# Kernel tuning notes

Measured on AMD Instinct MI355X. Metric: run time of the kernel, lower is better.

## Reference

```python
import jax, jax.numpy as jnp
import numpy as np

N = 100000   # nodes
E = 1600000  # edges
F_IN = 256   # nfeat
H = 64       # hidden_sizes
C = 40       # nclass


def gcn_norm(edge_index, edge_weight, num_nodes):
    # Add self-loops with weight 1 (PyG gcn_norm default fill_value=1.0)
    loop = jnp.arange(num_nodes)
    row = jnp.concatenate([edge_index[0], loop])
    col = jnp.concatenate([edge_index[1], loop])
    w = jnp.concatenate([edge_weight, jnp.ones((num_nodes,), edge_weight.dtype)])
    # Symmetric normalization: D^-1/2 A D^-1/2 (degree computed at target, per PyG)
    deg = jax.ops.segment_sum(w, col, num_segments=num_nodes)
    deg_inv_sqrt = jnp.where(deg > 0, jax.lax.rsqrt(deg), 0.0)
    norm = deg_inv_sqrt[row] * w * deg_inv_sqrt[col]
    return row, col, norm


def gcn_conv(x, W, b, row, col, norm, num_nodes):
    # Linear transform first (shrinks feature dim before irregular traffic)
    x = x @ W                                    # [N, out]
    msgs = norm[:, None] * x[row]                # gather + scale: [E+N, out]
    out = jax.ops.segment_sum(msgs, col, num_segments=num_nodes)  # scatter-add
    return out + b


def setup_inputs() -> dict:
    key = jax.random.key(0)
    k = jax.random.split(key, 7)
    x = jax.random.normal(k[0], (N, F_IN), dtype=jnp.float32)
    edge_index = jax.random.randint(k[1], (2, E), 0, N, dtype=jnp.int64)
    edge_attr = jax.random.uniform(k[2], (E,), dtype=jnp.float32)
    W1 = jax.random.normal(k[3], (F_IN, H), dtype=jnp.float32) * (1.0 / np.sqrt(F_IN))
    b1 = jnp.zeros((H,), jnp.float32)
    W2 = jax.random.normal(k[4], (H, C), dtype=jnp.float32) * (1.0 / np.sqrt(H))
    b2 = jnp.zeros((C,), jnp.float32)
    return {"x": x, "edge_index": edge_index, "edge_attr": edge_attr,
            "W1": W1, "b1": b1, "W2": W2, "b2": b2}


def reference(x, edge_index, edge_attr, W1, b1, W2, b2):
    row, col, norm = gcn_norm(edge_index, edge_attr, N)
    h = jax.nn.relu(gcn_conv(x, W1, b1, row, col, norm, N))
    # F.dropout with training=False is identity (eval mode)
    final = gcn_conv(h, W2, b2, row, col, norm, N)
    return final, jax.nn.log_softmax(final, axis=1)
```

## Files before the change

### kernel.cpp

```cpp
#include <hip/hip_runtime.h>
#include <hip/hip_bf16.h>
#include <math.h>

#define NN 100000
#define EE 1600000
#define FIN 256
#define HID 64
#define NC 40
#define NB 196
#define BCAP 10240
#define CHUNK 2048
#define NBKB ((EE + CHUNK - 1) / CHUNK)

typedef unsigned long long ull;
typedef __attribute__((ext_vector_type(2))) unsigned long long ullx2;
typedef __attribute__((ext_vector_type(8))) short short8;
typedef __attribute__((ext_vector_type(4))) float f32x4;

__device__ __forceinline__ unsigned short f2bf_rne(float f) {
    unsigned u = __float_as_uint(f);
    u += 0x7FFFu + ((u >> 16) & 1u);
    return (unsigned short)(u >> 16);
}
__device__ __forceinline__ float bf2f(unsigned short b) {
    return __uint_as_float((unsigned)b << 16);
}

__device__ __forceinline__ void edge_acc(ull q, const unsigned* __restrict__ tbl,
                                         int fl, float& a0, float& a1) {
    unsigned src = (unsigned)q & 0x1FFFFu;
    unsigned u = tbl[(src << 5) | fl];
    float w = __int_as_float((int)(q >> 32));
    a0 += w * __uint_as_float(u << 16);
    a1 += w * __uint_as_float(u & 0xFFFF0000u);
}

__global__ __launch_bounds__(256) void bucket_kernel(const int* __restrict__ row,
                                                     const int* __restrict__ col,
                                                     const float* __restrict__ w,
                                                     int* __restrict__ bucket_cnt,
                                                     int2* __restrict__ staging) {
    __shared__ int2 spay[CHUNK];
    __shared__ int2 sorted[CHUNK];
    __shared__ unsigned char sb[CHUNK];
    __shared__ unsigned char sbk[CHUNK];
    __shared__ int lcnt[NB], lofs[NB], lstart[NB];
    __shared__ int sscan[256];
    const int tid = threadIdx.x;
    const int e0 = blockIdx.x * CHUNK;
    const int nE = min(CHUNK, EE - e0);
    for (int i = tid; i < nE; i += 256) {
        int e = e0 + i;
        int c = col[e];
        sb[i] = (unsigned char)(c >> 9);
        spay[i] = make_int2(((c & 511) << 17) | row[e], __float_as_int(w[e]));
    }
    for (int i = tid; i < NB; i += 256) lcnt[i] = 0;
    __syncthreads();
    for (int i = tid; i < nE; i += 256) atomicAdd(&lcnt[sb[i]], 1);
    __syncthreads();
    int v = (tid < NB) ? lcnt[tid] : 0;
    sscan[tid] = v;
    __syncthreads();
    for (int off = 1; off < 256; off <<= 1) {
        int u = (tid >= off) ? sscan[tid - off] : 0;
        __syncthreads();
        sscan[tid] += u;
        __syncthreads();
    }
    if (tid < NB) {
        lofs[tid] = sscan[tid] - v;
        lstart[tid] = v ? atomicAdd(&bucket_cnt[tid], v) : 0;
        lcnt[tid] = 0;
    }
    __syncthreads();
    for (int i = tid; i < nE; i += 256) {
        int b = sb[i];
        int p = lofs[b] + atomicAdd(&lcnt[b], 1);
        sorted[p] = spay[i];
        sbk[p] = (unsigned char)b;
    }
    __syncthreads();
    for (int p = tid; p < nE; p += 256) {
        int b = sbk[p];
        int slot = lstart[b] + (p - lofs[b]);
        if (slot < BCAP) staging[(size_t)b * BCAP + slot] = sorted[p];
    }
}

__global__ __launch_bounds__(512) void build_count_kernel(const int2* __restrict__ staging,
                                                          const int* __restrict__ bucket_cnt,
                                                          int* __restrict__ basev,
                                                          int* __restrict__ endv,
                                                          float* __restrict__ dis,
                                                          int* __restrict__ ptot) {
    __shared__ int dcnt[512];
    __shared__ float dsum[512];
    __shared__ int sscan[512];
    const int t = threadIdx.x;
    const int b = blockIdx.x;
    const int nE = min(bucket_cnt[b], BCAP);
    const int2* st = staging + (size_t)b * BCAP;
    dcnt[t] = 0; dsum[t] = 0.f;
    __syncthreads();
    for (int i = t; i < nE; i += 512) {
        int2 p = st[i];
        int d = p.x >> 17;
        atomicAdd(&dcnt[d], 1);
        atomicAdd(&dsum[d], __int_as_float(p.y));
    }
    __syncthreads();
    int c = dcnt[t];
    int pdeg = (c + 7) & ~7;
    sscan[t] = pdeg;
    __syncthreads();
    for (int off = 1; off < 512; off <<= 1) {
        int u = (t >= off) ? sscan[t - off] : 0;
        __syncthreads();
        sscan[t] += u;
        __syncthreads();
    }
    int gd = b * 512 + t;
    if (gd < NN) {
        basev[gd] = sscan[t] - pdeg;
        endv[gd] = c;
        dis[gd] = rsqrtf(dsum[t] + 1.0f);
    }
    if (t == 511) ptot[b] = sscan[511];
}

__global__ __launch_bounds__(256) void bscan_w1cvt_kernel(const int* __restrict__ ptot,
                                                          int* __restrict__ bucket_base,
                                                          const float* __restrict__ W1,
                                                          unsigned short* __restrict__ w1hi,
                                                          unsigned short* __restrict__ w1lo) {
    if (blockIdx.x == 0) {
        __shared__ int sd[256];
        int t = threadIdx.x;
        int v = (t < NB) ? ptot[t] : 0;
        sd[t] = v;
        __syncthreads();
        for (int off = 1; off < 256; off <<= 1) {
            int u = (t >= off) ? sd[t - off] : 0;
            __syncthreads();
            sd[t] += u;
            __syncthreads();
        }
        if (t < NB) bucket_base[t] = sd[t] - v;
    } else {
        int b = blockIdx.x - 1;
        for (int i = threadIdx.x; i < 4096; i += 256) {
            int e = b * 4096 + i;
            int c = e >> 8, k = e & 255;
            float v = W1[(size_t)k * HID + c];
            unsigned short h = f2bf_rne(v);
            w1hi[e] = h;
            w1lo[e] = f2bf_rne(v - bf2f(h));
        }
    }
}

__global__ __launch_bounds__(512) void build_place_kernel(const int2* __restrict__ staging,
                                                          const int* __restrict__ bucket_cnt,
                                                          const int* __restrict__ bucket_base,
                                                          int* __restrict__ basev,
                                                          int* __restrict__ endv,
                                                          const float* __restrict__ dis,
                                                          int2* __restrict__ eme) {
    __shared__ int dcur[512];
    __shared__ float sdis[512];
    const int t = threadIdx.x;
    const int b = blockIdx.x;
    const int nE = min(bucket_cnt[b], BCAP);
    const int2* st = staging + (size_t)b * BCAP;
    const int gd = b * 512 + t;
    int gb = 0, c = 0, pdeg = 0;
    if (gd < NN) {
        gb = bucket_base[b] + basev[gd];
        c = endv[gd];
        pdeg = (c + 7) & ~7;
        basev[gd] = gb;
        endv[gd] = gb + c;
        sdis[t] = dis[gd];
    } else {
        sdis[t] = 0.f;
    }
    dcur[t] = gb;
    __syncthreads();
    for (int i = t; i < nE; i += 512) {
        int2 p = st[i];
        int d = p.x >> 17;
        int src = p.x & 0x1FFFF;
        int pos = atomicAdd(&dcur[d], 1);
        float wn = __int_as_float(p.y) * dis[src] * sdis[d];
        eme[pos] = make_int2(src, __float_as_int(wn));
    }
    for (int i = c; i < pdeg; i++) eme[gb + i] = make_int2(0, 0);
}

__global__ __launch_bounds__(512, 4) void gemm1_mfma_kernel(const float* __restrict__ x,
                                                            const unsigned short* __restrict__ w1hi,
                                                            const unsigned short* __restrict__ w1lo,
                                                            __hip_bfloat16* __restrict__ xw) {
    __shared__ unsigned short shi[4096 * 2];
    __shared__ unsigned short slo[4096 * 2];
    const int tid = threadIdx.x;
    const int wid = tid >> 6;
    const int l   = tid & 63;
    const int r   = l & 15;
    const int kg  = l >> 4;
    const int rb0 = blockIdx.x * 128 + wid * 16;

    f32x4 acc[4];
#pragma unroll
    for (int j = 0; j < 4; j++) acc[j] = (f32x4){0.f, 0.f, 0.f, 0.f};

    int row0 = rb0 + r;
    int row0c = row0 < NN ? row0 : NN - 1;
    const float* ap = x + (size_t)row0c * FIN + kg * 8;

#pragma unroll
    for (int ph = 0; ph < 2; ph++) {
        for (int c2 = tid; c2 < 1024; c2 += 512) {
            int ckg = c2 & 3, ccol = (c2 >> 2) & 63, cksl = c2 >> 8;
            size_t src = (size_t)ccol * FIN + (ph * 4 + cksl) * 32 + ckg * 8;
            int dst = ((cksl * 64 + ccol) * 32 + ckg * 8);
            *(short8*)(shi + dst) = *(const short8*)(w1hi + src);
            *(short8*)(slo + dst) = *(const short8*)(w1lo + src);
        }
        __syncthreads();
#pragma unroll
        for (int ksl = 0; ksl < 4; ksl++) {
            const int ks = ph * 4 + ksl;
            float4 afa = *(const float4*)(ap + ks * 32);
            float4 afb = *(const float4*)(ap + ks * 32 + 4);
            float av[8] = {afa.x, afa.y, afa.z, afa.w, afb.x, afb.y, afb.z, afb.w};
            short8 ahi, alo;
#pragma unroll
            for (int j = 0; j < 8; j++) {
                unsigned short hh = f2bf_rne(av[j]);
                ahi[j] = (short)hh;
                alo[j] = (short)f2bf_rne(av[j] - bf2f(hh));
            }
#pragma unroll
            for (int ct = 0; ct < 4; ct++) {
                int bo = ((ksl * 64 + ct * 16 + r) * 32 + kg * 8);
                short8 bh = *(const short8*)(shi + bo);
                short8 bl = *(const short8*)(slo + bo);
                acc[ct] = __builtin_amdgcn_mfma_f32_16x16x32_bf16(ahi, bh, acc[ct], 0, 0, 0);
                acc[ct] = __builtin_amdgcn_mfma_f32_16x16x32_bf16(ahi, bl, acc[ct], 0, 0, 0);
                acc[ct] = __builtin_amdgcn_mfma_f32_16x16x32_bf16(alo, bh, acc[ct], 0, 0, 0);
            }
        }
        __syncthreads();
    }
#pragma unroll
    for (int i = 0; i < 4; i++) {
        int grow = rb0 + kg * 4 + i;
        if (grow < NN) {
            unsigned short* dst = (unsigned short*)xw + (size_t)grow * HID + r;
#pragma unroll
            for (int ct = 0; ct < 4; ct++)
                dst[ct * 16] = f2bf_rne(acc[ct][i]);
        }
    }
}

__global__ __launch_bounds__(256) void gather1_kernel(const int* __restrict__ basev,
                                                      const int* __restrict__ endv,
                                                      const ull* __restrict__ eme,
                                                      const unsigned* __restrict__ xw32,
                                                      const float* __restrict__ dis,
                                                      const float* __restrict__ b,
                                                      float* __restrict__ h) {
    int n = blockIdx.x * 4 + (threadIdx.x >> 6);
    if (n >= NN) return;
    int lane = threadIdx.x & 63;
    int half = lane >> 5;
    int fl = lane & 31;
    int s = basev[n], t = endv[n];
    int pdeg = (t - s + 7) & ~7;
    float acc0 = 0.f, acc1 = 0.f;
    int nb16 = pdeg >> 4;
    for (int bi = 0; bi < nb16; bi++) {
        const ull* pp = eme + s + bi * 16 + 8 * half;
        ullx2 qa = *(const ullx2*)(pp);
        ullx2 qb = *(const ullx2*)(pp + 2);
        ullx2 qc = *(const ullx2*)(pp + 4);
        ullx2 qd = *(const ullx2*)(pp + 6);
        edge_acc(qa[0], xw32, fl, acc0, acc1);
        edge_acc(qa[1], xw32, fl, acc0, acc1);
        edge_acc(qb[0], xw32, fl, acc0, acc1);
        edge_acc(qb[1], xw32, fl, acc0, acc1);
        edge_acc(qc[0], xw32, fl, acc0, acc1);
        edge_acc(qc[1], xw32, fl, acc0, acc1);
        edge_acc(qd[0], xw32, fl, acc0, acc1);
        edge_acc(qd[1], xw32, fl, acc0, acc1);
    }
    if (pdeg & 8) {
        const ull* pp = eme + s + nb16 * 16 + 4 * half;
        ullx2 qa = *(const ullx2*)(pp);
        ullx2 qb = *(const ullx2*)(pp + 2);
        edge_acc(qa[0], xw32, fl, acc0, acc1);
        edge_acc(qa[1], xw32, fl, acc0, acc1);
        edge_acc(qb[0], xw32, fl, acc0, acc1);
        edge_acc(qb[1], xw32, fl, acc0, acc1);
    }
    acc0 += __shfl_xor(acc0, 32);
    acc1 += __shfl_xor(acc1, 32);
    float d = dis[n];
    unsigned un = xw32[((unsigned)n << 5) | fl];
    float2 bv = *(const float2*)(b + 2 * fl);
    float v0 = acc0 + d * d * __uint_as_float(un << 16) + bv.x;
    float v1 = acc1 + d * d * __uint_as_float(un & 0xFFFF0000u) + bv.y;
    if (lane < 32) {
        *(float2*)(h + (size_t)n * HID + 2 * fl) = make_float2(fmaxf(v0, 0.f), fmaxf(v1, 0.f));
    }
}

__global__ __launch_bounds__(256) void gemm2_kernel(const float* __restrict__ h,
                                                    const float* __restrict__ W,
                                                    __hip_bfloat16* __restrict__ hw) {
    __shared__ float hs[64][65];
    __shared__ float Ws[HID * NC];
    const int tid = threadIdx.x;
    const int base = blockIdx.x * 64;
    for (int v = tid; v < 1024; v += 256) {
        int r = v >> 4, q = v & 15;
        int gr = base + r;
        float4 hv = make_float4(0.f, 0.f, 0.f, 0.f);
        if (gr < NN) hv = *(const float4*)(h + (size_t)gr * HID + q * 4);
        hs[r][q * 4 + 0] = hv.x; hs[r][q * 4 + 1] = hv.y;
        hs[r][q * 4 + 2] = hv.z; hs[r][q * 4 + 3] = hv.w;
    }
    for (int v = tid; v < HID * NC; v += 256) Ws[v] = W[v];
    __syncthreads();
    const int tx = tid & 7;
    const int ty = tid >> 3;
    float acc[2][5] = {};
#pragma unroll 8
    for (int k = 0; k < HID; k++) {
        float h0 = hs[ty * 2 + 0][k];
        float h1 = hs[ty * 2 + 1][k];
        const float* wr = &Ws[k * NC + tx * 5];
        float w0 = wr[0], w1 = wr[1], w2 = wr[2], w3 = wr[3], w4 = wr[4];
        acc[0][0] += h0 * w0; acc[0][1] += h0 * w1; acc[0][2] += h0 * w2;
        acc[0][3] += h0 * w3; acc[0][4] += h0 * w4;
        acc[1][0] += h1 * w0; acc[1][1] += h1 * w1; acc[1][2] += h1 * w2;
        acc[1][3] += h1 * w3; acc[1][4] += h1 * w4;
    }
#pragma unroll
    for (int i = 0; i < 2; i++) {
        int gr = base + ty * 2 + i;
        if (gr < NN) {
#pragma unroll
            for (int c = 0; c < 5; c++)
                hw[(size_t)gr * 64 + tx * 5 + c] = __float2bfloat16(acc[i][c]);
        }
    }
}

__global__ __launch_bounds__(256) void gather2_kernel(const int* __restrict__ basev,
                                                      const int* __restrict__ endv,
                                                      const ull* __restrict__ eme,
                                                      const unsigned* __restrict__ hw32,
                                                      const float* __restrict__ dis,
                                                      const float* __restrict__ b,
                                                      float* __restrict__ out) {
    int n = blockIdx.x * 4 + (threadIdx.x >> 6);
    if (n >= NN) return;
    int lane = threadIdx.x & 63;
    int half = lane >> 5;
    int fl = lane & 31;
    bool act = fl < 20;
    int s = basev[n], t = endv[n];
    int pdeg = (t - s + 7) & ~7;
    float acc0 = 0.f, acc1 = 0.f;
    int nb16 = pdeg >> 4;
    for (int bi = 0; bi < nb16; bi++) {
        const ull* pp = eme + s + bi * 16 + 8 * half;
        ullx2 qa = *(const ullx2*)(pp);
        ullx2 qb = *(const ullx2*)(pp + 2);
        ullx2 qc = *(const ullx2*)(pp + 4);
        ullx2 qd = *(const ullx2*)(pp + 6);
        edge_acc(qa[0], hw32, fl, acc0, acc1);
        edge_acc(qa[1], hw32, fl, acc0, acc1);
        edge_acc(qb[0], hw32, fl, acc0, acc1);
        edge_acc(qb[1], hw32, fl, acc0, acc1);
        edge_acc(qc[0], hw32, fl, acc0, acc1);
        edge_acc(qc[1], hw32, fl, acc0, acc1);
        edge_acc(qd[0], hw32, fl, acc0, acc1);
        edge_acc(qd[1], hw32, fl, acc0, acc1);
    }
    if (pdeg & 8) {
        const ull* pp = eme + s + nb16 * 16 + 4 * half;
        ullx2 qa = *(const ullx2*)(pp);
        ullx2 qb = *(const ullx2*)(pp + 2);
        edge_acc(qa[0], hw32, fl, acc0, acc1);
        edge_acc(qa[1], hw32, fl, acc0, acc1);
        edge_acc(qb[0], hw32, fl, acc0, acc1);
        edge_acc(qb[1], hw32, fl, acc0, acc1);
    }
    acc0 += __shfl_xor(acc0, 32);
    acc1 += __shfl_xor(acc1, 32);
    float v0 = 0.f, v1 = 0.f, m = -INFINITY;
    if (act) {
        float d = dis[n];
        unsigned un = hw32[((unsigned)n << 5) | fl];
        float2 bv = *(const float2*)(b + 2 * fl);
        v0 = acc0 + d * d * __uint_as_float(un << 16) + bv.x;
        v1 = acc1 + d * d * __uint_as_float(un & 0xFFFF0000u) + bv.y;
        m = fmaxf(v0, v1);
    }
#pragma unroll
    for (int off = 16; off; off >>= 1) m = fmaxf(m, __shfl_xor(m, off));
    float e0 = act ? expf(v0 - m) : 0.f;
    float e1 = act ? expf(v1 - m) : 0.f;
    float sum = e0 + e1;
#pragma unroll
    for (int off = 16; off; off >>= 1) sum += __shfl_xor(sum, off);
    float lse = m + logf(sum);
    if (act && lane < 32) {
        size_t idx = (size_t)n * NC + 2 * fl;
        *(float2*)(out + idx) = make_float2(v0, v1);
        *(float2*)(out + (size_t)NN * NC + idx) = make_float2(v0 - lse, v1 - lse);
    }
}

extern "C" void kernel_launch(void* const* d_in, const int* in_sizes, int n_in,
                              void* d_out, int out_size, void* d_ws, size_t ws_size,
                              hipStream_t stream) {
    const float* x    = (const float*)d_in[0];
    const int*   eidx = (const int*)d_in[1];
    const float* ew   = (const float*)d_in[2];
    const float* W1   = (const float*)d_in[3];
    const float* b1   = (const float*)d_in[4];
    const float* W2   = (const float*)d_in[5];
    const float* b2   = (const float*)d_in[6];
    float* out = (float*)d_out;

    const int* row = eidx;
    const int* col = eidx + EE;

    char* ws = (char*)d_ws;
    int*   bucket_cnt  = (int*)ws;               ws += 256 * 4;
    int*   bucket_base = (int*)ws;               ws += 256 * 4;
    int*   ptot        = (int*)ws;               ws += 256 * 4;
    float* dis    = (float*)ws;                  ws += NN * 4;
    int*   basev  = (int*)ws;                    ws += NN * 4;
    int*   endv   = (int*)ws;                    ws += NN * 4;
    int2*  eme    = (int2*)ws;                   ws += ((size_t)EE + 8 * NN) * 8;
    __hip_bfloat16* xw = (__hip_bfloat16*)ws;    ws += (size_t)NN * HID * 2;
    char* unionp = ws;                           ws += (size_t)NN * HID * 4;
    int2*  staging = (int2*)unionp;
    float* h       = (float*)unionp;
    __hip_bfloat16* hw2 = (__hip_bfloat16*)ws;   ws += (size_t)NN * 64 * 2;
    unsigned short* w1hi = (unsigned short*)ws;  ws += (size_t)HID * FIN * 2;
    unsigned short* w1lo = (unsigned short*)ws;  ws += (size_t)HID * FIN * 2;

    hipMemsetAsync(bucket_cnt, 0, 256 * 4, stream);

    bucket_kernel<<<NBKB, 256, 0, stream>>>(row, col, ew, bucket_cnt, staging);
    build_count_kernel<<<NB, 512, 0, stream>>>(staging, bucket_cnt,
                                               basev, endv, dis, ptot);
    bscan_w1cvt_kernel<<<5, 256, 0, stream>>>(ptot, bucket_base, W1, w1hi, w1lo);
    build_place_kernel<<<NB, 512, 0, stream>>>(staging, bucket_cnt, bucket_base,
                                               basev, endv, dis, eme);
    gemm1_mfma_kernel<<<(NN + 127) / 128, 512, 0, stream>>>(x, w1hi, w1lo, xw);
    gather1_kernel<<<(NN + 3) / 4, 256, 0, stream>>>(basev, endv, (const ull*)eme,
                                                     (const unsigned*)xw, dis, b1, h);
    gemm2_kernel<<<(NN + 63) / 64, 256, 0, stream>>>(h, W2, hw2);
    gather2_kernel<<<(NN + 3) / 4, 256, 0, stream>>>(basev, endv, (const ull*)eme,
                                                     (const unsigned*)hw2, dis, b2, out);
}
```

Before: 357.5 us.

## Fuse edge bucketing with GEMM1 and replace bucket-base scan with atomic offsets

```diff
diff --git a/kernel.cpp b/kernel.cpp
--- a/kernel.cpp
+++ b/kernel.cpp
@@ -11,6 +11,7 @@
 #define BCAP 10240
 #define CHUNK 2048
 #define NBKB ((EE + CHUNK - 1) / CHUNK)
+#define NGEMM ((NN + 127) / 128)
 
 typedef unsigned long long ull;
 typedef __attribute__((ext_vector_type(2))) unsigned long long ullx2;
@@ -35,56 +36,133 @@
     a1 += w * __uint_as_float(u & 0xFFFF0000u);
 }
 
-__global__ __launch_bounds__(256) void bucket_kernel(const int* __restrict__ row,
-                                                     const int* __restrict__ col,
-                                                     const float* __restrict__ w,
-                                                     int* __restrict__ bucket_cnt,
-                                                     int2* __restrict__ staging) {
-    __shared__ int2 spay[CHUNK];
-    __shared__ int2 sorted[CHUNK];
-    __shared__ unsigned char sb[CHUNK];
-    __shared__ unsigned char sbk[CHUNK];
-    __shared__ int lcnt[NB], lofs[NB], lstart[NB];
-    __shared__ int sscan[256];
+__global__ __launch_bounds__(512, 4) void fused_bucket_gemm1_kernel(
+        const int* __restrict__ row, const int* __restrict__ col,
+        const float* __restrict__ w, int* __restrict__ bucket_cnt,
+        int2* __restrict__ staging,
+        const float* __restrict__ x, const float* __restrict__ W1,
+        __hip_bfloat16* __restrict__ xw) {
+    __shared__ __align__(16) unsigned char smem[40960];
     const int tid = threadIdx.x;
-    const int e0 = blockIdx.x * CHUNK;
-    const int nE = min(CHUNK, EE - e0);
-    for (int i = tid; i < nE; i += 256) {
-        int e = e0 + i;
-        int c = col[e];
-        sb[i] = (unsigned char)(c >> 9);
-        spay[i] = make_int2(((c & 511) << 17) | row[e], __float_as_int(w[e]));
-    }
-    for (int i = tid; i < NB; i += 256) lcnt[i] = 0;
-    __syncthreads();
-    for (int i = tid; i < nE; i += 256) atomicAdd(&lcnt[sb[i]], 1);
-    __syncthreads();
-    int v = (tid < NB) ? lcnt[tid] : 0;
-    sscan[tid] = v;
-    __syncthreads();
-    for (int off = 1; off < 256; off <<= 1) {
-        int u = (tid >= off) ? sscan[tid - off] : 0;
-        __syncthreads();
-        sscan[tid] += u;
-        __syncthreads();
-    }
-    if (tid < NB) {
-        lofs[tid] = sscan[tid] - v;
-        lstart[tid] = v ? atomicAdd(&bucket_cnt[tid], v) : 0;
-        lcnt[tid] = 0;
-    }
-    __syncthreads();
-    for (int i = tid; i < nE; i += 256) {
-        int b = sb[i];
-        int p = lofs[b] + atomicAdd(&lcnt[b], 1);
-        sorted[p] = spay[i];
-        sbk[p] = (unsigned char)b;
-    }
-    __syncthreads();
-    for (int p = tid; p < nE; p += 256) {
-        int b = sbk[p];
-        int slot = lstart[b] + (p - lofs[b]);
-        if (slot < BCAP) staging[(size_t)b * BCAP + slot] = sorted[p];
+
+    if (blockIdx.x < NBKB) {
+        int2* spay   = (int2*)(smem);
+        int2* sorted = (int2*)(smem + 16384);
+        unsigned char* sb  = smem + 32768;
+        unsigned char* sbk = smem + 34816;
+        int* lcnt   = (int*)(smem + 36864);
+        int* lofs   = (int*)(smem + 37648);
+        int* lstart = (int*)(smem + 38432);
+        int* sscan  = (int*)(smem + 39216);
+        const int e0 = blockIdx.x * CHUNK;
+        const int nE = min(CHUNK, EE - e0);
+        for (int i = tid; i < nE; i += 512) {
+            int e = e0 + i;
+            int c = col[e];
+            sb[i] = (unsigned char)(c >> 9);
+            spay[i] = make_int2(((c & 511) << 17) | row[e], __float_as_int(w[e]));
+        }
+        for (int i = tid; i < NB; i += 512) lcnt[i] = 0;
+        __syncthreads();
+        for (int i = tid; i < nE; i += 512) atomicAdd(&lcnt[sb[i]], 1);
+        __syncthreads();
+        int v = (tid < NB) ? lcnt[tid] : 0;
+        if (tid < 256) sscan[tid] = v;
+        __syncthreads();
+        for (int off = 1; off < 256; off <<= 1) {
+            int u = (tid >= off && tid < 256) ? sscan[tid - off] : 0;
+            __syncthreads();
+            if (tid < 256) sscan[tid] += u;
+            __syncthreads();
+        }
+        if (tid < NB) {
+            lofs[tid] = sscan[tid] - v;
+            lstart[tid] = v ? atomicAdd(&bucket_cnt[tid], v) : 0;
+            lcnt[tid] = 0;
+        }
+        __syncthreads();
+        for (int i = tid; i < nE; i += 512) {
+            int b = sb[i];
+            int p = lofs[b] + atomicAdd(&lcnt[b], 1);
+            sorted[p] = spay[i];
+            sbk[p] = (unsigned char)b;
+        }
+        __syncthreads();
+        for (int p = tid; p < nE; p += 512) {
+            int b = sbk[p];
+            int slot = lstart[b] + (p - lofs[b]);
+            if (slot < BCAP) staging[(size_t)b * BCAP + slot] = sorted[p];
+        }
+    } else {
+        unsigned short* shi = (unsigned short*)(smem);
+        unsigned short* slo = (unsigned short*)(smem + 16384);
+        const int wid = tid >> 6;
+        const int l   = tid & 63;
+        const int r   = l & 15;
+        const int kg  = l >> 4;
+        const int rb0 = (blockIdx.x - NBKB) * 128 + wid * 16;
+
+        f32x4 acc[4];
+#pragma unroll
+        for (int j = 0; j < 4; j++) acc[j] = (f32x4){0.f, 0.f, 0.f, 0.f};
+
+        int row0 = rb0 + r;
+        int row0c = row0 < NN ? row0 : NN - 1;
+        const float* ap = x + (size_t)row0c * FIN + kg * 8;
+
+#pragma unroll
+        for (int ph = 0; ph < 2; ph++) {
+            for (int c2 = tid; c2 < 1024; c2 += 512) {
+                int ckg = c2 & 3, ccol = (c2 >> 2) & 63, cksl = c2 >> 8;
+                int kb = (ph * 4 + cksl) * 32 + ckg * 8;
+                short8 vh, vl;
+#pragma unroll
+                for (int j = 0; j < 8; j++) {
+                    float v = W1[(size_t)(kb + j) * HID + ccol];
+                    unsigned short hh = f2bf_rne(v);
+                    vh[j] = (short)hh;
+                    vl[j] = (short)f2bf_rne(v - bf2f(hh));
+                }
+                int dst = (cksl * 64 + ccol) * 32 + ckg * 8;
+                *(short8*)(shi + dst) = vh;
+                *(short8*)(slo + dst) = vl;
+            }
+            __syncthreads();
+#pragma unroll
+            for (int ksl = 0; ksl < 4; ksl++) {
+                const int ks = ph * 4 + ksl;
+                float4 afa = *(const float4*)(ap + ks * 32);
+                float4 afb = *(const float4*)(ap + ks * 32 + 4);
+                float av[8] = {afa.x, afa.y, afa.z, afa.w, afb.x, afb.y, afb.z, afb.w};
+                short8 ahi, alo;
+#pragma unroll
+                for (int j = 0; j < 8; j++) {
+                    unsigned short hh = f2bf_rne(av[j]);
+                    ahi[j] = (short)hh;
+                    alo[j] = (short)f2bf_rne(av[j] - bf2f(hh));
+                }
+#pragma unroll
+                for (int ct = 0; ct < 4; ct++) {
+                    int bo = (ksl * 64 + ct * 16 + r) * 32 + kg * 8;
+                    short8 bh = *(const short8*)(shi + bo);
+                    short8 bl = *(const short8*)(slo + bo);
+                    acc[ct] = __builtin_amdgcn_mfma_f32_16x16x32_bf16(ahi, bh, acc[ct], 0, 0, 0);
+                    acc[ct] = __builtin_amdgcn_mfma_f32_16x16x32_bf16(ahi, bl, acc[ct], 0, 0, 0);
+                    acc[ct] = __builtin_amdgcn_mfma_f32_16x16x32_bf16(alo, bh, acc[ct], 0, 0, 0);
+                }
+            }
+            __syncthreads();
+        }
+#pragma unroll
+        for (int i = 0; i < 4; i++) {
+            int grow = rb0 + kg * 4 + i;
+            if (grow < NN) {
+                unsigned short* dst = (unsigned short*)xw + (size_t)grow * HID + r;
+#pragma unroll
+                for (int ct = 0; ct < 4; ct++)
+                    dst[ct * 16] = f2bf_rne(acc[ct][i]);
+            }
+        }
     }
 }
 
@@ -93,10 +171,11 @@
                                                           int* __restrict__ basev,
                                                           int* __restrict__ endv,
                                                           float* __restrict__ dis,
-                                                          int* __restrict__ ptot) {
+                                                          int* __restrict__ gcnt) {
     __shared__ int dcnt[512];
     __shared__ float dsum[512];
     __shared__ int sscan[512];
+    __shared__ int bbase;
     const int t = threadIdx.x;
     const int b = blockIdx.x;
     const int nE = min(bucket_cnt[b], BCAP);
@@ -120,51 +199,21 @@
         sscan[t] += u;
         __syncthreads();
     }
+    if (t == 511) bbase = atomicAdd(gcnt, sscan[511]);
+    __syncthreads();
+    int gb = bbase + sscan[t] - pdeg;
     int gd = b * 512 + t;
     if (gd < NN) {
-        basev[gd] = sscan[t] - pdeg;
-        endv[gd] = c;
+        basev[gd] = gb;
+        endv[gd] = gb + c;
         dis[gd] = rsqrtf(dsum[t] + 1.0f);
-    }
-    if (t == 511) ptot[b] = sscan[511];
-}
-
-__global__ __launch_bounds__(256) void bscan_w1cvt_kernel(const int* __restrict__ ptot,
-                                                          int* __restrict__ bucket_base,
-                                                          const float* __restrict__ W1,
-                                                          unsigned short* __restrict__ w1hi,
-                                                          unsigned short* __restrict__ w1lo) {
-    if (blockIdx.x == 0) {
-        __shared__ int sd[256];
-        int t = threadIdx.x;
-        int v = (t < NB) ? ptot[t] : 0;
-        sd[t] = v;
-        __syncthreads();
-        for (int off = 1; off < 256; off <<= 1) {
-            int u = (t >= off) ? sd[t - off] : 0;
-            __syncthreads();
-            sd[t] += u;
-            __syncthreads();
-        }
-        if (t < NB) bucket_base[t] = sd[t] - v;
-    } else {
-        int b = blockIdx.x - 1;
-        for (int i = threadIdx.x; i < 4096; i += 256) {
-            int e = b * 4096 + i;
-            int c = e >> 8, k = e & 255;
-            float v = W1[(size_t)k * HID + c];
-            unsigned short h = f2bf_rne(v);
-            w1hi[e] = h;
-            w1lo[e] = f2bf_rne(v - bf2f(h));
-        }
     }
 }
 
 __global__ __launch_bounds__(512) void build_place_kernel(const int2* __restrict__ staging,
                                                           const int* __restrict__ bucket_cnt,
-                                                          const int* __restrict__ bucket_base,
-                                                          int* __restrict__ basev,
-                                                          int* __restrict__ endv,
+                                                          const int* __restrict__ basev,
+                                                          const int* __restrict__ endv,
                                                           const float* __restrict__ dis,
                                                           int2* __restrict__ eme) {
     __shared__ int dcur[512];
@@ -176,11 +225,9 @@
     const int gd = b * 512 + t;
     int gb = 0, c = 0, pdeg = 0;
     if (gd < NN) {
-        gb = bucket_base[b] + basev[gd];
-        c = endv[gd];
+        gb = basev[gd];
+        c = endv[gd] - gb;
         pdeg = (c + 7) & ~7;
-        basev[gd] = gb;
-        endv[gd] = gb + c;
         sdis[t] = dis[gd];
     } else {
         sdis[t] = 0.f;
@@ -196,74 +243,6 @@
         eme[pos] = make_int2(src, __float_as_int(wn));
     }
     for (int i = c; i < pdeg; i++) eme[gb + i] = make_int2(0, 0);
-}
-
-__global__ __launch_bounds__(512, 4) void gemm1_mfma_kernel(const float* __restrict__ x,
-                                                            const unsigned short* __restrict__ w1hi,
-                                                            const unsigned short* __restrict__ w1lo,
-                                                            __hip_bfloat16* __restrict__ xw) {
-    __shared__ unsigned short shi[4096 * 2];
-    __shared__ unsigned short slo[4096 * 2];
-    const int tid = threadIdx.x;
-    const int wid = tid >> 6;
-    const int l   = tid & 63;
-    const int r   = l & 15;
-    const int kg  = l >> 4;
-    const int rb0 = blockIdx.x * 128 + wid * 16;
-
-    f32x4 acc[4];
-#pragma unroll
-    for (int j = 0; j < 4; j++) acc[j] = (f32x4){0.f, 0.f, 0.f, 0.f};
-
-    int row0 = rb0 + r;
-    int row0c = row0 < NN ? row0 : NN - 1;
-    const float* ap = x + (size_t)row0c * FIN + kg * 8;
-
-#pragma unroll
-    for (int ph = 0; ph < 2; ph++) {
-        for (int c2 = tid; c2 < 1024; c2 += 512) {
-            int ckg = c2 & 3, ccol = (c2 >> 2) & 63, cksl = c2 >> 8;
-            size_t src = (size_t)ccol * FIN + (ph * 4 + cksl) * 32 + ckg * 8;
-            int dst = ((cksl * 64 + ccol) * 32 + ckg * 8);
-            *(short8*)(shi + dst) = *(const short8*)(w1hi + src);
-            *(short8*)(slo + dst) = *(const short8*)(w1lo + src);
-        }
-        __syncthreads();
-#pragma unroll
-        for (int ksl = 0; ksl < 4; ksl++) {
-            const int ks = ph * 4 + ksl;
-            float4 afa = *(const float4*)(ap + ks * 32);
-            float4 afb = *(const float4*)(ap + ks * 32 + 4);
-            float av[8] = {afa.x, afa.y, afa.z, afa.w, afb.x, afb.y, afb.z, afb.w};
-            short8 ahi, alo;
-#pragma unroll
-            for (int j = 0; j < 8; j++) {
-                unsigned short hh = f2bf_rne(av[j]);
-                ahi[j] = (short)hh;
-                alo[j] = (short)f2bf_rne(av[j] - bf2f(hh));
-            }
-#pragma unroll
-            for (int ct = 0; ct < 4; ct++) {
-                int bo = ((ksl * 64 + ct * 16 + r) * 32 + kg * 8);
-                short8 bh = *(const short8*)(shi + bo);
-                short8 bl = *(const short8*)(slo + bo);
-                acc[ct] = __builtin_amdgcn_mfma_f32_16x16x32_bf16(ahi, bh, acc[ct], 0, 0, 0);
-                acc[ct] = __builtin_amdgcn_mfma_f32_16x16x32_bf16(ahi, bl, acc[ct], 0, 0, 0);
-                acc[ct] = __builtin_amdgcn_mfma_f32_16x16x32_bf16(alo, bh, acc[ct], 0, 0, 0);
-            }
-        }
-        __syncthreads();
-    }
-#pragma unroll
-    for (int i = 0; i < 4; i++) {
-        int grow = rb0 + kg * 4 + i;
-        if (grow < NN) {
-            unsigned short* dst = (unsigned short*)xw + (size_t)grow * HID + r;
-#pragma unroll
-            for (int ct = 0; ct < 4; ct++)
-                dst[ct * 16] = f2bf_rne(acc[ct][i]);
-        }
-    }
 }
 
 __global__ __launch_bounds__(256) void gather1_kernel(const int* __restrict__ basev,
@@ -444,8 +423,7 @@
 
     char* ws = (char*)d_ws;
     int*   bucket_cnt  = (int*)ws;               ws += 256 * 4;
-    int*   bucket_base = (int*)ws;               ws += 256 * 4;
-    int*   ptot        = (int*)ws;               ws += 256 * 4;
+    int*   gcnt        = (int*)ws;               ws += 64 * 4;
     float* dis    = (float*)ws;                  ws += NN * 4;
     int*   basev  = (int*)ws;                    ws += NN * 4;
     int*   endv   = (int*)ws;                    ws += NN * 4;
@@ -455,18 +433,15 @@
     int2*  staging = (int2*)unionp;
     float* h       = (float*)unionp;
     __hip_bfloat16* hw2 = (__hip_bfloat16*)ws;   ws += (size_t)NN * 64 * 2;
-    unsigned short* w1hi = (unsigned short*)ws;  ws += (size_t)HID * FIN * 2;
-    unsigned short* w1lo = (unsigned short*)ws;  ws += (size_t)HID * FIN * 2;
-
-    hipMemsetAsync(bucket_cnt, 0, 256 * 4, stream);
-
-    bucket_kernel<<<NBKB, 256, 0, stream>>>(row, col, ew, bucket_cnt, staging);
+
+    hipMemsetAsync(bucket_cnt, 0, 256 * 4 + 64 * 4, stream);
+
+    fused_bucket_gemm1_kernel<<<NBKB + NGEMM, 512, 0, stream>>>(
+        row, col, ew, bucket_cnt, staging, x, W1, xw);
     build_count_kernel<<<NB, 512, 0, stream>>>(staging, bucket_cnt,
-                                               basev, endv, dis, ptot);
-    bscan_w1cvt_kernel<<<5, 256, 0, stream>>>(ptot, bucket_base, W1, w1hi, w1lo);
-    build_place_kernel<<<NB, 512, 0, stream>>>(staging, bucket_cnt, bucket_base,
+                                               basev, endv, dis, gcnt);
+    build_place_kernel<<<NB, 512, 0, stream>>>(staging, bucket_cnt,
                                                basev, endv, dis, eme);
-    gemm1_mfma_kernel<<<(NN + 127) / 128, 512, 0, stream>>>(x, w1hi, w1lo, xw);
     gather1_kernel<<<(NN + 3) / 4, 256, 0, stream>>>(basev, endv, (const ull*)eme,
                                                      (const unsigned*)xw, dis, b1, h);
     gemm2_kernel<<<(NN + 63) / 64, 256, 0, stream>>>(h, W2, hw2);
```

New measurement: 350.2 us. 1.02x faster.
